# Kernel tuning notes

Measured on AMD Instinct MI355X. Metric: run time of the kernel, lower is better.

## Reference

```python
import jax, jax.numpy as jnp
import numpy as np

ALPHA = 500.0
BETA = 0.5
DEGREE = 20
LAMBDA_MAX = 100.0
N_USERS = 50000
N_ITEMS = 20000
NNZ = 2_000_000
BATCH = 128


def _aspire_filter(lam):
    exponent = 2.0 - BETA
    lam_pow = np.power(np.maximum(lam, 0.0), exponent / 2.0)
    return lam_pow / (lam_pow + ALPHA)


def _compute_chebyshev_coeffs(lambda_min, lambda_max, K):
    j = np.arange(K + 1)
    theta = np.pi * (j + 0.5) / (K + 1)
    t_nodes = np.cos(theta)
    mid, half = (lambda_max + lambda_min) / 2.0, (lambda_max - lambda_min) / 2.0
    f_nodes = _aspire_filter(mid + half * t_nodes)
    coeffs = np.zeros(K + 1)
    for k in range(K + 1):
        coeffs[k] = 2.0 / (K + 1) * np.sum(f_nodes * np.cos(k * theta))
    coeffs[0] /= 2.0
    return coeffs.astype(np.float32)


def setup_inputs() -> dict:
    key = jax.random.key(0)
    k1, k2, k3, k4 = jax.random.split(key, 4)
    rows = jax.random.randint(k1, (NNZ,), 0, N_USERS).astype(jnp.int32)
    cols = jax.random.randint(k2, (NNZ,), 0, N_ITEMS).astype(jnp.int32)
    vals = jax.random.uniform(k3, (NNZ,), dtype=jnp.float32)
    X_batch = jax.random.normal(k4, (BATCH, N_ITEMS), dtype=jnp.float32)
    coeffs = jnp.asarray(_compute_chebyshev_coeffs(0.0, LAMBDA_MAX, DEGREE))
    t_mid = jnp.full((1,), LAMBDA_MAX / 2.0, dtype=jnp.float32)
    t_half = jnp.full((1,), LAMBDA_MAX / 2.0, dtype=jnp.float32)
    return {
        "X_batch": X_batch,
        "vals": vals,
        "coeffs": coeffs,
        "t_mid": t_mid,
        "t_half": t_half,
        "rows": rows,
        "cols": cols,
        "n_users": N_USERS,
    }


def reference(X_batch, vals, coeffs, t_mid, t_half, rows, cols, n_users):
    n_items = X_batch.shape[1]

    def S_mapped(v):  # v: [n_items, batch]
        # X @ v : gather item rows, scatter-add into users
        u = jax.ops.segment_sum(vals[:, None] * v[cols], rows, num_segments=n_users)
        # X^T @ u : gather user rows, scatter-add into items
        w = jax.ops.segment_sum(vals[:, None] * u[rows], cols, num_segments=n_items)
        return (w - t_mid * v) / t_half

    T_prev = X_batch.T  # [n_items, batch]
    T_curr = S_mapped(T_prev)
    out0 = coeffs[0] * T_prev + coeffs[1] * T_curr

    def step(carry, c):
        Tp, Tc, acc = carry
        Tn = 2.0 * S_mapped(Tc) - Tp
        return (Tc, Tn, acc + c * Tn), None

    (_, _, out), _ = jax.lax.scan(step, (T_prev, T_curr, out0), coeffs[2:])
    return out.T  # [batch, n_items]
```

## Files before the change

### kernel.cpp

```cpp
#include <hip/hip_runtime.h>

#define BATCH 128
#define NUSERS 50000

__global__ void hist_k(const int* __restrict__ keys, int* __restrict__ hist, int nnz) {
  int i = blockIdx.x * blockDim.x + threadIdx.x;
  int st = gridDim.x * blockDim.x;
  for (; i < nnz; i += st) atomicAdd(&hist[keys[i]], 1);
}

__global__ void scan_k(const int* __restrict__ hist, int* __restrict__ offs,
                       int* __restrict__ cursor, int n) {
  __shared__ int wsum[16];
  __shared__ int carry;
  int tid = threadIdx.x;
  int lane = tid & 63;
  int wv = tid >> 6;
  if (tid == 0) carry = 0;
  __syncthreads();
  for (int base = 0; base < n; base += 1024) {
    int i = base + tid;
    int x = (i < n) ? hist[i] : 0;
    int incl = x;
#pragma unroll
    for (int d = 1; d < 64; d <<= 1) {
      int y = __shfl_up(incl, (unsigned)d, 64);
      if (lane >= d) incl += y;
    }
    if (lane == 63) wsum[wv] = incl;
    __syncthreads();
    if (wv == 0) {
      int t = (lane < 16) ? wsum[lane] : 0;
#pragma unroll
      for (int d = 1; d < 16; d <<= 1) {
        int y = __shfl_up(t, (unsigned)d, 64);
        if (lane >= d) t += y;
      }
      if (lane < 16) wsum[lane] = t;
    }
    __syncthreads();
    int woff = (wv > 0) ? wsum[wv - 1] : 0;
    int excl = carry + woff + incl - x;
    if (i < n) { offs[i] = excl; cursor[i] = excl; }
    int chunk_total = wsum[15];
    __syncthreads();
    if (tid == 0) carry += chunk_total;
    __syncthreads();
  }
  if (tid == 0) offs[n] = carry;
}

__global__ void scatter_k(const int* __restrict__ keys, const int* __restrict__ other,
                          const float* __restrict__ vals, int* __restrict__ cursor,
                          int2* __restrict__ out_ev, int nnz) {
  int i = blockIdx.x * blockDim.x + threadIdx.x;
  int st = gridDim.x * blockDim.x;
  for (; i < nnz; i += st) {
    int k = keys[i];
    int p = atomicAdd(&cursor[k], 1);
    out_ev[p] = make_int2(other[i], __float_as_int(vals[i]));
  }
}

__global__ void transpose_init_k(const float* __restrict__ Xb, const float* __restrict__ coeffs,
                                 float* __restrict__ T0, float* __restrict__ acc, int nitems) {
  __shared__ float tile[32][33];
  int tx = threadIdx.x, ty = threadIdx.y;
  int i0 = blockIdx.x * 32, b0 = blockIdx.y * 32;
#pragma unroll
  for (int j = 0; j < 4; j++) {
    int b = b0 + ty + j * 8;
    tile[ty + j * 8][tx] = Xb[(size_t)b * nitems + i0 + tx];
  }
  __syncthreads();
  float c0 = coeffs[0];
#pragma unroll
  for (int j = 0; j < 4; j++) {
    int il = ty + j * 8;
    float v = tile[tx][il];
    size_t idx = (size_t)(i0 + il) * BATCH + b0 + tx;
    T0[idx] = v;
    acc[idx] = c0 * v;
  }
}

__global__ void transpose_out_k(const float* __restrict__ acc, float* __restrict__ out, int nitems) {
  __shared__ float tile[32][33];
  int tx = threadIdx.x, ty = threadIdx.y;
  int i0 = blockIdx.x * 32, b0 = blockIdx.y * 32;
#pragma unroll
  for (int j = 0; j < 4; j++) {
    int il = ty + j * 8;
    tile[il][tx] = acc[(size_t)(i0 + il) * BATCH + b0 + tx];
  }
  __syncthreads();
#pragma unroll
  for (int j = 0; j < 4; j++) {
    int bl = ty + j * 8;
    out[(size_t)(b0 + bl) * nitems + i0 + tx] = tile[tx][bl];
  }
}

__global__ void __launch_bounds__(256) spmm_u_k(const int* __restrict__ offs,
                                                const int2* __restrict__ ev,
                                                const float* __restrict__ v,
                                                float* __restrict__ u, int nrows) {
  int row = (blockIdx.x << 2) | (threadIdx.x >> 6);
  if (row >= nrows) return;
  int lane = threadIdx.x & 63;
  int k0 = offs[row], k1 = offs[row + 1];
  float2 a0 = {0.f, 0.f}, a1 = {0.f, 0.f}, a2 = {0.f, 0.f}, a3 = {0.f, 0.f};
  int k = k0;
  int co = lane << 1;
  for (; k + 4 <= k1; k += 4) {
    int2 e0 = ev[k], e1 = ev[k + 1], e2 = ev[k + 2], e3 = ev[k + 3];
    float2 x0 = *reinterpret_cast<const float2*>(v + ((size_t)e0.x << 7) + co);
    float2 x1 = *reinterpret_cast<const float2*>(v + ((size_t)e1.x << 7) + co);
    float2 x2 = *reinterpret_cast<const float2*>(v + ((size_t)e2.x << 7) + co);
    float2 x3 = *reinterpret_cast<const float2*>(v + ((size_t)e3.x << 7) + co);
    float w0 = __int_as_float(e0.y), w1 = __int_as_float(e1.y);
    float w2 = __int_as_float(e2.y), w3 = __int_as_float(e3.y);
    a0.x = fmaf(w0, x0.x, a0.x); a0.y = fmaf(w0, x0.y, a0.y);
    a1.x = fmaf(w1, x1.x, a1.x); a1.y = fmaf(w1, x1.y, a1.y);
    a2.x = fmaf(w2, x2.x, a2.x); a2.y = fmaf(w2, x2.y, a2.y);
    a3.x = fmaf(w3, x3.x, a3.x); a3.y = fmaf(w3, x3.y, a3.y);
  }
  for (; k < k1; ++k) {
    int2 e = ev[k];
    float2 x = *reinterpret_cast<const float2*>(v + ((size_t)e.x << 7) + co);
    float w = __int_as_float(e.y);
    a0.x = fmaf(w, x.x, a0.x); a0.y = fmaf(w, x.y, a0.y);
  }
  float2 s;
  s.x = (a0.x + a1.x) + (a2.x + a3.x);
  s.y = (a0.y + a1.y) + (a2.y + a3.y);
  *reinterpret_cast<float2*>(u + ((size_t)row << 7) + co) = s;
}

__global__ void __launch_bounds__(256) spmm_i_cheb_k(const int* __restrict__ offs,
                                                     const int2* __restrict__ ev,
                                                     const float* __restrict__ u,
                                                     const float* __restrict__ vcur,
                                                     float* __restrict__ tio,
                                                     float* __restrict__ acc,
                                                     const float* __restrict__ t_mid,
                                                     const float* __restrict__ t_half,
                                                     const float* __restrict__ coeffs,
                                                     int cix, float sA, float sB, int nitems) {
  int item = (blockIdx.x << 2) | (threadIdx.x >> 6);
  if (item >= nitems) return;
  int lane = threadIdx.x & 63;
  int k0 = offs[item], k1 = offs[item + 1];
  float2 a0 = {0.f, 0.f}, a1 = {0.f, 0.f}, a2 = {0.f, 0.f}, a3 = {0.f, 0.f};
  int k = k0;
  int co = lane << 1;
  for (; k + 4 <= k1; k += 4) {
    int2 e0 = ev[k], e1 = ev[k + 1], e2 = ev[k + 2], e3 = ev[k + 3];
    float2 x0 = *reinterpret_cast<const float2*>(u + ((size_t)e0.x << 7) + co);
    float2 x1 = *reinterpret_cast<const float2*>(u + ((size_t)e1.x << 7) + co);
    float2 x2 = *reinterpret_cast<const float2*>(u + ((size_t)e2.x << 7) + co);
    float2 x3 = *reinterpret_cast<const float2*>(u + ((size_t)e3.x << 7) + co);
    float w0 = __int_as_float(e0.y), w1 = __int_as_float(e1.y);
    float w2 = __int_as_float(e2.y), w3 = __int_as_float(e3.y);
    a0.x = fmaf(w0, x0.x, a0.x); a0.y = fmaf(w0, x0.y, a0.y);
    a1.x = fmaf(w1, x1.x, a1.x); a1.y = fmaf(w1, x1.y, a1.y);
    a2.x = fmaf(w2, x2.x, a2.x); a2.y = fmaf(w2, x2.y, a2.y);
    a3.x = fmaf(w3, x3.x, a3.x); a3.y = fmaf(w3, x3.y, a3.y);
  }
  for (; k < k1; ++k) {
    int2 e = ev[k];
    float2 x = *reinterpret_cast<const float2*>(u + ((size_t)e.x << 7) + co);
    float w = __int_as_float(e.y);
    a0.x = fmaf(w, x.x, a0.x); a0.y = fmaf(w, x.y, a0.y);
  }
  float2 w;
  w.x = (a0.x + a1.x) + (a2.x + a3.x);
  w.y = (a0.y + a1.y) + (a2.y + a3.y);

  float mid = t_mid[0];
  float inv = 1.0f / t_half[0];
  float c = coeffs[cix];
  size_t idx = ((size_t)item << 7) + co;
  float2 vv = *reinterpret_cast<const float2*>(vcur + idx);
  float2 t;
  t.x = (w.x - mid * vv.x) * inv;
  t.y = (w.y - mid * vv.y) * inv;
  if (sB != 0.0f) {
    float2 p = *reinterpret_cast<const float2*>(tio + idx);
    t.x = sA * t.x - sB * p.x;
    t.y = sA * t.y - sB * p.y;
  }
  *reinterpret_cast<float2*>(tio + idx) = t;
  float2 a = *reinterpret_cast<const float2*>(acc + idx);
  a.x = fmaf(c, t.x, a.x);
  a.y = fmaf(c, t.y, a.y);
  *reinterpret_cast<float2*>(acc + idx) = a;
}

extern "C" void kernel_launch(void* const* d_in, const int* in_sizes, int n_in,
                              void* d_out, int out_size, void* d_ws, size_t ws_size,
                              hipStream_t stream) {
  const float* Xb     = (const float*)d_in[0];
  const float* vals   = (const float*)d_in[1];
  const float* coeffs = (const float*)d_in[2];
  const float* t_mid  = (const float*)d_in[3];
  const float* t_half = (const float*)d_in[4];
  const int*   rows   = (const int*)d_in[5];
  const int*   cols   = (const int*)d_in[6];

  int nnz    = in_sizes[1];
  int nitems = in_sizes[0] / BATCH;
  int nusers = NUSERS;
  int ncoef  = in_sizes[2];

  char* base = (char*)d_ws;
  size_t o = 0;
  auto alloc = [&](size_t bytes) -> void* {
    void* p = base + o;
    o = (o + bytes + 255) & ~(size_t)255;
    return p;
  };
  int2*  csr_ev   = (int2*)alloc((size_t)nnz * 8);
  int*   csr_offs = (int*)alloc((size_t)(nusers + 1) * 4);
  int2*  csc_ev   = (int2*)alloc((size_t)nnz * 8);
  int*   csc_offs = (int*)alloc((size_t)(nitems + 1) * 4);
  int*   cursor   = (int*)alloc((size_t)(nusers + 1) * 4);
  int*   hist     = (int*)alloc((size_t)(nusers + 1) * 4);
  float* u        = (float*)alloc((size_t)nusers * BATCH * 4);
  float* Ta       = (float*)alloc((size_t)nitems * BATCH * 4);
  float* Tb       = (float*)alloc((size_t)nitems * BATCH * 4);
  float* accb     = (float*)alloc((size_t)nitems * BATCH * 4);
  (void)ws_size;

  hipMemsetAsync(hist, 0, (size_t)(nusers + 1) * 4, stream);
  hist_k<<<2048, 256, 0, stream>>>(rows, hist, nnz);
  scan_k<<<1, 1024, 0, stream>>>(hist, csr_offs, cursor, nusers);
  scatter_k<<<2048, 256, 0, stream>>>(rows, cols, vals, cursor, csr_ev, nnz);

  hipMemsetAsync(hist, 0, (size_t)(nusers + 1) * 4, stream);
  hist_k<<<2048, 256, 0, stream>>>(cols, hist, nnz);
  scan_k<<<1, 1024, 0, stream>>>(hist, csc_offs, cursor, nitems);
  scatter_k<<<2048, 256, 0, stream>>>(cols, rows, vals, cursor, csc_ev, nnz);

  dim3 tb(32, 8);
  transpose_init_k<<<dim3(nitems / 32, BATCH / 32), tb, 0, stream>>>(Xb, coeffs, Ta, accb, nitems);

  int ublocks = (nusers + 3) / 4;
  int iblocks = (nitems + 3) / 4;

  spmm_u_k<<<ublocks, 256, 0, stream>>>(csr_offs, csr_ev, Ta, u, nusers);
  spmm_i_cheb_k<<<iblocks, 256, 0, stream>>>(csc_offs, csc_ev, u, Ta, Tb, accb,
                                             t_mid, t_half, coeffs, 1, 1.0f, 0.0f, nitems);
  float* Tp = Ta;
  float* Tc = Tb;
  for (int s = 2; s < ncoef; ++s) {
    spmm_u_k<<<ublocks, 256, 0, stream>>>(csr_offs, csr_ev, Tc, u, nusers);
    spmm_i_cheb_k<<<iblocks, 256, 0, stream>>>(csc_offs, csc_ev, u, Tc, Tp, accb,
                                               t_mid, t_half, coeffs, s, 2.0f, 1.0f, nitems);
    float* tmp = Tp; Tp = Tc; Tc = tmp;
  }

  transpose_out_k<<<dim3(nitems / 32, BATCH / 32), tb, 0, stream>>>(accb, (float*)d_out, nitems);
}
```

Measured before the change: 5.400 ms.

## Build CSR from CSC and rebuild CSC from CSR for locality, prefetch edges

The CSR is now built by rescattering a column-sorted COO, so each user's edges end up ordered by item. The CSC is then rebuilt from that CSR so each item's edges are ordered by user. Neighbouring gathers in the SpMM kernels should hit nearby rows of the dense operand, which improves cache locality. The SpMM loops also software-prefetch the next four edge entries and make the wave index uniform with readfirstlane. The cost is more preprocessing passes with atomics, plus reuse of the u buffer as scratch during setup.

Result: faster. 5.054 ms (-6.4%).

```diff
diff --git a/kernel.cpp b/kernel.cpp
--- a/kernel.cpp
+++ b/kernel.cpp
@@ -50,15 +50,34 @@
   if (tid == 0) offs[n] = carry;
 }
 
-__global__ void scatter_k(const int* __restrict__ keys, const int* __restrict__ other,
-                          const float* __restrict__ vals, int* __restrict__ cursor,
-                          int2* __restrict__ out_ev, int nnz) {
+__global__ void reinit_cursor_k(const int* __restrict__ offs, int* __restrict__ cursor, int n) {
+  int i = blockIdx.x * blockDim.x + threadIdx.x;
+  if (i < n) cursor[i] = offs[i];
+}
+
+__global__ void scatter1_k(const int* __restrict__ rows, const int* __restrict__ cols,
+                           const float* __restrict__ vals, int* __restrict__ cursor,
+                           int2* __restrict__ out_ev, int* __restrict__ keycomp, int nnz) {
   int i = blockIdx.x * blockDim.x + threadIdx.x;
   int st = gridDim.x * blockDim.x;
   for (; i < nnz; i += st) {
-    int k = keys[i];
-    int p = atomicAdd(&cursor[k], 1);
-    out_ev[p] = make_int2(other[i], __float_as_int(vals[i]));
+    int c = cols[i];
+    int p = atomicAdd(&cursor[c], 1);
+    out_ev[p] = make_int2(rows[i], __float_as_int(vals[i]));
+    keycomp[p] = c;
+  }
+}
+
+__global__ void rescatter_k(const int2* __restrict__ in_ev, const int* __restrict__ in_comp,
+                            int* __restrict__ cursor, int2* __restrict__ out_ev,
+                            int* __restrict__ out_comp, int nnz) {
+  int i = blockIdx.x * blockDim.x + threadIdx.x;
+  int st = gridDim.x * blockDim.x;
+  for (; i < nnz; i += st) {
+    int2 e = in_ev[i];
+    int q = atomicAdd(&cursor[e.x], 1);
+    out_ev[q] = make_int2(in_comp[i], e.y);
+    if (out_comp) out_comp[q] = e.x;
   }
 }
 
@@ -105,21 +124,27 @@
                                                 const int2* __restrict__ ev,
                                                 const float* __restrict__ v,
                                                 float* __restrict__ u, int nrows) {
-  int row = (blockIdx.x << 2) | (threadIdx.x >> 6);
+  int wid = __builtin_amdgcn_readfirstlane(threadIdx.x >> 6);
+  int row = (blockIdx.x << 2) | wid;
   if (row >= nrows) return;
   int lane = threadIdx.x & 63;
+  int co = lane << 1;
   int k0 = offs[row], k1 = offs[row + 1];
   float2 a0 = {0.f, 0.f}, a1 = {0.f, 0.f}, a2 = {0.f, 0.f}, a3 = {0.f, 0.f};
   int k = k0;
-  int co = lane << 1;
-  for (; k + 4 <= k1; k += 4) {
-    int2 e0 = ev[k], e1 = ev[k + 1], e2 = ev[k + 2], e3 = ev[k + 3];
+  int2 e0, e1, e2, e3;
+  bool have = (k + 4 <= k1);
+  if (have) { e0 = ev[k]; e1 = ev[k + 1]; e2 = ev[k + 2]; e3 = ev[k + 3]; }
+  while (have) {
     float2 x0 = *reinterpret_cast<const float2*>(v + ((size_t)e0.x << 7) + co);
     float2 x1 = *reinterpret_cast<const float2*>(v + ((size_t)e1.x << 7) + co);
     float2 x2 = *reinterpret_cast<const float2*>(v + ((size_t)e2.x << 7) + co);
     float2 x3 = *reinterpret_cast<const float2*>(v + ((size_t)e3.x << 7) + co);
     float w0 = __int_as_float(e0.y), w1 = __int_as_float(e1.y);
     float w2 = __int_as_float(e2.y), w3 = __int_as_float(e3.y);
+    k += 4;
+    have = (k + 4 <= k1);
+    if (have) { e0 = ev[k]; e1 = ev[k + 1]; e2 = ev[k + 2]; e3 = ev[k + 3]; }
     a0.x = fmaf(w0, x0.x, a0.x); a0.y = fmaf(w0, x0.y, a0.y);
     a1.x = fmaf(w1, x1.x, a1.x); a1.y = fmaf(w1, x1.y, a1.y);
     a2.x = fmaf(w2, x2.x, a2.x); a2.y = fmaf(w2, x2.y, a2.y);
@@ -147,21 +172,27 @@
                                                      const float* __restrict__ t_half,
                                                      const float* __restrict__ coeffs,
                                                      int cix, float sA, float sB, int nitems) {
-  int item = (blockIdx.x << 2) | (threadIdx.x >> 6);
+  int wid = __builtin_amdgcn_readfirstlane(threadIdx.x >> 6);
+  int item = (blockIdx.x << 2) | wid;
   if (item >= nitems) return;
   int lane = threadIdx.x & 63;
+  int co = lane << 1;
   int k0 = offs[item], k1 = offs[item + 1];
   float2 a0 = {0.f, 0.f}, a1 = {0.f, 0.f}, a2 = {0.f, 0.f}, a3 = {0.f, 0.f};
   int k = k0;
-  int co = lane << 1;
-  for (; k + 4 <= k1; k += 4) {
-    int2 e0 = ev[k], e1 = ev[k + 1], e2 = ev[k + 2], e3 = ev[k + 3];
+  int2 e0, e1, e2, e3;
+  bool have = (k + 4 <= k1);
+  if (have) { e0 = ev[k]; e1 = ev[k + 1]; e2 = ev[k + 2]; e3 = ev[k + 3]; }
+  while (have) {
     float2 x0 = *reinterpret_cast<const float2*>(u + ((size_t)e0.x << 7) + co);
     float2 x1 = *reinterpret_cast<const float2*>(u + ((size_t)e1.x << 7) + co);
     float2 x2 = *reinterpret_cast<const float2*>(u + ((size_t)e2.x << 7) + co);
     float2 x3 = *reinterpret_cast<const float2*>(u + ((size_t)e3.x << 7) + co);
     float w0 = __int_as_float(e0.y), w1 = __int_as_float(e1.y);
     float w2 = __int_as_float(e2.y), w3 = __int_as_float(e3.y);
+    k += 4;
+    have = (k + 4 <= k1);
+    if (have) { e0 = ev[k]; e1 = ev[k + 1]; e2 = ev[k + 2]; e3 = ev[k + 3]; }
     a0.x = fmaf(w0, x0.x, a0.x); a0.y = fmaf(w0, x0.y, a0.y);
     a1.x = fmaf(w1, x1.x, a1.x); a1.y = fmaf(w1, x1.y, a1.y);
     a2.x = fmaf(w2, x2.x, a2.x); a2.y = fmaf(w2, x2.y, a2.y);
@@ -220,9 +251,9 @@
     o = (o + bytes + 255) & ~(size_t)255;
     return p;
   };
+  int2*  csc_ev   = (int2*)alloc((size_t)nnz * 8);
   int2*  csr_ev   = (int2*)alloc((size_t)nnz * 8);
   int*   csr_offs = (int*)alloc((size_t)(nusers + 1) * 4);
-  int2*  csc_ev   = (int2*)alloc((size_t)nnz * 8);
   int*   csc_offs = (int*)alloc((size_t)(nitems + 1) * 4);
   int*   cursor   = (int*)alloc((size_t)(nusers + 1) * 4);
   int*   hist     = (int*)alloc((size_t)(nusers + 1) * 4);
@@ -231,16 +262,22 @@
   float* Tb       = (float*)alloc((size_t)nitems * BATCH * 4);
   float* accb     = (float*)alloc((size_t)nitems * BATCH * 4);
   (void)ws_size;
+  int* comp_a = (int*)u;
+  int* comp_b = ((int*)u) + nnz;
+
+  hipMemsetAsync(hist, 0, (size_t)(nusers + 1) * 4, stream);
+  hist_k<<<2048, 256, 0, stream>>>(cols, hist, nnz);
+  scan_k<<<1, 1024, 0, stream>>>(hist, csc_offs, cursor, nitems);
+  int2* csc_tmp = csc_ev;
+  scatter1_k<<<2048, 256, 0, stream>>>(rows, cols, vals, cursor, csc_tmp, comp_a, nnz);
 
   hipMemsetAsync(hist, 0, (size_t)(nusers + 1) * 4, stream);
   hist_k<<<2048, 256, 0, stream>>>(rows, hist, nnz);
   scan_k<<<1, 1024, 0, stream>>>(hist, csr_offs, cursor, nusers);
-  scatter_k<<<2048, 256, 0, stream>>>(rows, cols, vals, cursor, csr_ev, nnz);
-
-  hipMemsetAsync(hist, 0, (size_t)(nusers + 1) * 4, stream);
-  hist_k<<<2048, 256, 0, stream>>>(cols, hist, nnz);
-  scan_k<<<1, 1024, 0, stream>>>(hist, csc_offs, cursor, nitems);
-  scatter_k<<<2048, 256, 0, stream>>>(cols, rows, vals, cursor, csc_ev, nnz);
+  rescatter_k<<<2048, 256, 0, stream>>>(csc_tmp, comp_a, cursor, csr_ev, comp_b, nnz);
+
+  reinit_cursor_k<<<(nitems + 255) / 256, 256, 0, stream>>>(csc_offs, cursor, nitems);
+  rescatter_k<<<2048, 256, 0, stream>>>(csr_ev, comp_b, cursor, csc_ev, (int*)nullptr, nnz);
 
   dim3 tb(32, 8);
   transpose_init_k<<<dim3(nitems / 32, BATCH / 32), tb, 0, stream>>>(Xb, coeffs, Ta, accb, nitems);
```

## Split batch into 16-column slices and map 8 lanes per row in SpMM

Applied to the files above, without the earlier changes.

Dense operands are re-laid out as eight 16-wide batch slices, so each SpMM block works on one slice and the gathered rows form a working set small enough for cache. Each row is handled by 8 lanes that share edge indices through shuffles, replacing one 64-lane wavefront per row, which raises parallelism for short rows. CSR and CSC construction are also fused into single histogram and scatter passes. The cost is eight times more gather passes over the edge lists, each fetching only 64-byte segments.

Result: faster. 4.896 ms (-9.3%).

```diff
diff --git a/kernel.cpp b/kernel.cpp
--- a/kernel.cpp
+++ b/kernel.cpp
@@ -2,11 +2,17 @@
 
 #define BATCH 128
 #define NUSERS 50000
-
-__global__ void hist_k(const int* __restrict__ keys, int* __restrict__ hist, int nnz) {
+#define PW 16
+#define NSL 8
+
+__global__ void hist2_k(const int* __restrict__ rows, const int* __restrict__ cols,
+                        int* __restrict__ histU, int* __restrict__ histI, int nnz) {
   int i = blockIdx.x * blockDim.x + threadIdx.x;
   int st = gridDim.x * blockDim.x;
-  for (; i < nnz; i += st) atomicAdd(&hist[keys[i]], 1);
+  for (; i < nnz; i += st) {
+    atomicAdd(&histU[rows[i]], 1);
+    atomicAdd(&histI[cols[i]], 1);
+  }
 }
 
 __global__ void scan_k(const int* __restrict__ hist, int* __restrict__ offs,
@@ -50,91 +56,76 @@
   if (tid == 0) offs[n] = carry;
 }
 
-__global__ void scatter_k(const int* __restrict__ keys, const int* __restrict__ other,
-                          const float* __restrict__ vals, int* __restrict__ cursor,
-                          int2* __restrict__ out_ev, int nnz) {
+__global__ void scatter2_k(const int* __restrict__ rows, const int* __restrict__ cols,
+                           const float* __restrict__ vals, int* __restrict__ curU,
+                           int* __restrict__ curI, int2* __restrict__ csr_ev,
+                           int2* __restrict__ csc_ev, int nnz) {
   int i = blockIdx.x * blockDim.x + threadIdx.x;
   int st = gridDim.x * blockDim.x;
   for (; i < nnz; i += st) {
-    int k = keys[i];
-    int p = atomicAdd(&cursor[k], 1);
-    out_ev[p] = make_int2(other[i], __float_as_int(vals[i]));
+    int r = rows[i], c = cols[i];
+    int vb = __float_as_int(vals[i]);
+    int p = atomicAdd(&curU[r], 1);
+    csr_ev[p] = make_int2(c, vb);
+    int q = atomicAdd(&curI[c], 1);
+    csc_ev[q] = make_int2(r, vb);
   }
 }
 
 __global__ void transpose_init_k(const float* __restrict__ Xb, const float* __restrict__ coeffs,
                                  float* __restrict__ T0, float* __restrict__ acc, int nitems) {
-  __shared__ float tile[32][33];
+  __shared__ float t[16][17];
   int tx = threadIdx.x, ty = threadIdx.y;
-  int i0 = blockIdx.x * 32, b0 = blockIdx.y * 32;
-#pragma unroll
-  for (int j = 0; j < 4; j++) {
-    int b = b0 + ty + j * 8;
-    tile[ty + j * 8][tx] = Xb[(size_t)b * nitems + i0 + tx];
-  }
+  int p = blockIdx.y;
+  int i0 = blockIdx.x * 16;
+  t[ty][tx] = Xb[(size_t)(p * 16 + ty) * nitems + i0 + tx];
   __syncthreads();
   float c0 = coeffs[0];
-#pragma unroll
-  for (int j = 0; j < 4; j++) {
-    int il = ty + j * 8;
-    float v = tile[tx][il];
-    size_t idx = (size_t)(i0 + il) * BATCH + b0 + tx;
-    T0[idx] = v;
-    acc[idx] = c0 * v;
-  }
+  float v = t[tx][ty];
+  size_t o = (size_t)p * nitems * PW + (size_t)(i0 + ty) * PW + tx;
+  T0[o] = v;
+  acc[o] = c0 * v;
 }
 
 __global__ void transpose_out_k(const float* __restrict__ acc, float* __restrict__ out, int nitems) {
-  __shared__ float tile[32][33];
+  __shared__ float t[16][17];
   int tx = threadIdx.x, ty = threadIdx.y;
-  int i0 = blockIdx.x * 32, b0 = blockIdx.y * 32;
-#pragma unroll
-  for (int j = 0; j < 4; j++) {
-    int il = ty + j * 8;
-    tile[il][tx] = acc[(size_t)(i0 + il) * BATCH + b0 + tx];
-  }
+  int p = blockIdx.y;
+  int i0 = blockIdx.x * 16;
+  t[ty][tx] = acc[(size_t)p * nitems * PW + (size_t)(i0 + ty) * PW + tx];
   __syncthreads();
-#pragma unroll
-  for (int j = 0; j < 4; j++) {
-    int bl = ty + j * 8;
-    out[(size_t)(b0 + bl) * nitems + i0 + tx] = tile[tx][bl];
-  }
+  out[(size_t)(p * 16 + ty) * nitems + i0 + tx] = t[tx][ty];
 }
 
 __global__ void __launch_bounds__(256) spmm_u_k(const int* __restrict__ offs,
                                                 const int2* __restrict__ ev,
                                                 const float* __restrict__ v,
-                                                float* __restrict__ u, int nrows) {
-  int row = (blockIdx.x << 2) | (threadIdx.x >> 6);
+                                                float* __restrict__ u,
+                                                int nrows, size_t vstride, size_t ustride) {
+  int s = blockIdx.x & 7;
+  int g = blockIdx.x >> 3;
+  int slot = threadIdx.x >> 3;
+  int lane8 = threadIdx.x & 7;
+  int row = g * 32 + slot;
   if (row >= nrows) return;
-  int lane = threadIdx.x & 63;
   int k0 = offs[row], k1 = offs[row + 1];
-  float2 a0 = {0.f, 0.f}, a1 = {0.f, 0.f}, a2 = {0.f, 0.f}, a3 = {0.f, 0.f};
-  int k = k0;
-  int co = lane << 1;
-  for (; k + 4 <= k1; k += 4) {
-    int2 e0 = ev[k], e1 = ev[k + 1], e2 = ev[k + 2], e3 = ev[k + 3];
-    float2 x0 = *reinterpret_cast<const float2*>(v + ((size_t)e0.x << 7) + co);
-    float2 x1 = *reinterpret_cast<const float2*>(v + ((size_t)e1.x << 7) + co);
-    float2 x2 = *reinterpret_cast<const float2*>(v + ((size_t)e2.x << 7) + co);
-    float2 x3 = *reinterpret_cast<const float2*>(v + ((size_t)e3.x << 7) + co);
-    float w0 = __int_as_float(e0.y), w1 = __int_as_float(e1.y);
-    float w2 = __int_as_float(e2.y), w3 = __int_as_float(e3.y);
-    a0.x = fmaf(w0, x0.x, a0.x); a0.y = fmaf(w0, x0.y, a0.y);
-    a1.x = fmaf(w1, x1.x, a1.x); a1.y = fmaf(w1, x1.y, a1.y);
-    a2.x = fmaf(w2, x2.x, a2.x); a2.y = fmaf(w2, x2.y, a2.y);
-    a3.x = fmaf(w3, x3.x, a3.x); a3.y = fmaf(w3, x3.y, a3.y);
-  }
-  for (; k < k1; ++k) {
-    int2 e = ev[k];
-    float2 x = *reinterpret_cast<const float2*>(v + ((size_t)e.x << 7) + co);
-    float w = __int_as_float(e.y);
-    a0.x = fmaf(w, x.x, a0.x); a0.y = fmaf(w, x.y, a0.y);
-  }
-  float2 s;
-  s.x = (a0.x + a1.x) + (a2.x + a3.x);
-  s.y = (a0.y + a1.y) + (a2.y + a3.y);
-  *reinterpret_cast<float2*>(u + ((size_t)row << 7) + co) = s;
+  const float* vp = v + (size_t)s * vstride + (lane8 << 1);
+  float2 a = {0.f, 0.f};
+  int base = threadIdx.x & ~7;
+  for (int k = k0; k < k1; k += 8) {
+    int kk = k + lane8;
+    int2 e = (kk < k1) ? ev[kk] : make_int2(0, 0);
+#pragma unroll
+    for (int j = 0; j < 8; j++) {
+      int src = base | j;
+      int idx = __shfl(e.x, src);
+      float w = __int_as_float(__shfl(e.y, src));
+      float2 x = *reinterpret_cast<const float2*>(vp + ((size_t)idx << 4));
+      a.x = fmaf(w, x.x, a.x);
+      a.y = fmaf(w, x.y, a.y);
+    }
+  }
+  *reinterpret_cast<float2*>(u + (size_t)s * ustride + ((size_t)row << 4) + (lane8 << 1)) = a;
 }
 
 __global__ void __launch_bounds__(256) spmm_i_cheb_k(const int* __restrict__ offs,
@@ -146,41 +137,35 @@
                                                      const float* __restrict__ t_mid,
                                                      const float* __restrict__ t_half,
                                                      const float* __restrict__ coeffs,
-                                                     int cix, float sA, float sB, int nitems) {
-  int item = (blockIdx.x << 2) | (threadIdx.x >> 6);
+                                                     int cix, float sA, float sB,
+                                                     int nitems, size_t ustride, size_t tstride) {
+  int s = blockIdx.x & 7;
+  int g = blockIdx.x >> 3;
+  int slot = threadIdx.x >> 3;
+  int lane8 = threadIdx.x & 7;
+  int item = g * 32 + slot;
   if (item >= nitems) return;
-  int lane = threadIdx.x & 63;
   int k0 = offs[item], k1 = offs[item + 1];
-  float2 a0 = {0.f, 0.f}, a1 = {0.f, 0.f}, a2 = {0.f, 0.f}, a3 = {0.f, 0.f};
-  int k = k0;
-  int co = lane << 1;
-  for (; k + 4 <= k1; k += 4) {
-    int2 e0 = ev[k], e1 = ev[k + 1], e2 = ev[k + 2], e3 = ev[k + 3];
-    float2 x0 = *reinterpret_cast<const float2*>(u + ((size_t)e0.x << 7) + co);
-    float2 x1 = *reinterpret_cast<const float2*>(u + ((size_t)e1.x << 7) + co);
-    float2 x2 = *reinterpret_cast<const float2*>(u + ((size_t)e2.x << 7) + co);
-    float2 x3 = *reinterpret_cast<const float2*>(u + ((size_t)e3.x << 7) + co);
-    float w0 = __int_as_float(e0.y), w1 = __int_as_float(e1.y);
-    float w2 = __int_as_float(e2.y), w3 = __int_as_float(e3.y);
-    a0.x = fmaf(w0, x0.x, a0.x); a0.y = fmaf(w0, x0.y, a0.y);
-    a1.x = fmaf(w1, x1.x, a1.x); a1.y = fmaf(w1, x1.y, a1.y);
-    a2.x = fmaf(w2, x2.x, a2.x); a2.y = fmaf(w2, x2.y, a2.y);
-    a3.x = fmaf(w3, x3.x, a3.x); a3.y = fmaf(w3, x3.y, a3.y);
-  }
-  for (; k < k1; ++k) {
-    int2 e = ev[k];
-    float2 x = *reinterpret_cast<const float2*>(u + ((size_t)e.x << 7) + co);
-    float w = __int_as_float(e.y);
-    a0.x = fmaf(w, x.x, a0.x); a0.y = fmaf(w, x.y, a0.y);
-  }
-  float2 w;
-  w.x = (a0.x + a1.x) + (a2.x + a3.x);
-  w.y = (a0.y + a1.y) + (a2.y + a3.y);
-
+  const float* up = u + (size_t)s * ustride + (lane8 << 1);
+  float2 w = {0.f, 0.f};
+  int base = threadIdx.x & ~7;
+  for (int k = k0; k < k1; k += 8) {
+    int kk = k + lane8;
+    int2 e = (kk < k1) ? ev[kk] : make_int2(0, 0);
+#pragma unroll
+    for (int j = 0; j < 8; j++) {
+      int src = base | j;
+      int idx = __shfl(e.x, src);
+      float wv = __int_as_float(__shfl(e.y, src));
+      float2 x = *reinterpret_cast<const float2*>(up + ((size_t)idx << 4));
+      w.x = fmaf(wv, x.x, w.x);
+      w.y = fmaf(wv, x.y, w.y);
+    }
+  }
   float mid = t_mid[0];
   float inv = 1.0f / t_half[0];
   float c = coeffs[cix];
-  size_t idx = ((size_t)item << 7) + co;
+  size_t idx = (size_t)s * tstride + ((size_t)item << 4) + (lane8 << 1);
   float2 vv = *reinterpret_cast<const float2*>(vcur + idx);
   float2 t;
   t.x = (w.x - mid * vv.x) * inv;
@@ -213,6 +198,9 @@
   int nusers = NUSERS;
   int ncoef  = in_sizes[2];
 
+  size_t vstride = (size_t)nitems * PW;
+  size_t ustride = (size_t)nusers * PW;
+
   char* base = (char*)d_ws;
   size_t o = 0;
   auto alloc = [&](size_t bytes) -> void* {
@@ -221,44 +209,45 @@
     return p;
   };
   int2*  csr_ev   = (int2*)alloc((size_t)nnz * 8);
+  int2*  csc_ev   = (int2*)alloc((size_t)nnz * 8);
   int*   csr_offs = (int*)alloc((size_t)(nusers + 1) * 4);
-  int2*  csc_ev   = (int2*)alloc((size_t)nnz * 8);
   int*   csc_offs = (int*)alloc((size_t)(nitems + 1) * 4);
-  int*   cursor   = (int*)alloc((size_t)(nusers + 1) * 4);
-  int*   hist     = (int*)alloc((size_t)(nusers + 1) * 4);
-  float* u        = (float*)alloc((size_t)nusers * BATCH * 4);
-  float* Ta       = (float*)alloc((size_t)nitems * BATCH * 4);
-  float* Tb       = (float*)alloc((size_t)nitems * BATCH * 4);
-  float* accb     = (float*)alloc((size_t)nitems * BATCH * 4);
+  int*   curU     = (int*)alloc((size_t)(nusers + 1) * 4);
+  int*   curI     = (int*)alloc((size_t)(nitems + 1) * 4);
+  int*   histU    = (int*)alloc((size_t)(nusers + 1) * 4);
+  int*   histI    = (int*)alloc((size_t)(nitems + 1) * 4);
+  float* u        = (float*)alloc((size_t)NSL * ustride * 4);
+  float* Ta       = (float*)alloc((size_t)NSL * vstride * 4);
+  float* Tb       = (float*)alloc((size_t)NSL * vstride * 4);
+  float* accb     = (float*)alloc((size_t)NSL * vstride * 4);
   (void)ws_size;
 
-  hipMemsetAsync(hist, 0, (size_t)(nusers + 1) * 4, stream);
-  hist_k<<<2048, 256, 0, stream>>>(rows, hist, nnz);
-  scan_k<<<1, 1024, 0, stream>>>(hist, csr_offs, cursor, nusers);
-  scatter_k<<<2048, 256, 0, stream>>>(rows, cols, vals, cursor, csr_ev, nnz);
-
-  hipMemsetAsync(hist, 0, (size_t)(nusers + 1) * 4, stream);
-  hist_k<<<2048, 256, 0, stream>>>(cols, hist, nnz);
-  scan_k<<<1, 1024, 0, stream>>>(hist, csc_offs, cursor, nitems);
-  scatter_k<<<2048, 256, 0, stream>>>(cols, rows, vals, cursor, csc_ev, nnz);
-
-  dim3 tb(32, 8);
-  transpose_init_k<<<dim3(nitems / 32, BATCH / 32), tb, 0, stream>>>(Xb, coeffs, Ta, accb, nitems);
-
-  int ublocks = (nusers + 3) / 4;
-  int iblocks = (nitems + 3) / 4;
-
-  spmm_u_k<<<ublocks, 256, 0, stream>>>(csr_offs, csr_ev, Ta, u, nusers);
+  hipMemsetAsync(histU, 0, (size_t)(nusers + 1) * 4, stream);
+  hipMemsetAsync(histI, 0, (size_t)(nitems + 1) * 4, stream);
+  hist2_k<<<2048, 256, 0, stream>>>(rows, cols, histU, histI, nnz);
+  scan_k<<<1, 1024, 0, stream>>>(histU, csr_offs, curU, nusers);
+  scan_k<<<1, 1024, 0, stream>>>(histI, csc_offs, curI, nitems);
+  scatter2_k<<<2048, 256, 0, stream>>>(rows, cols, vals, curU, curI, csr_ev, csc_ev, nnz);
+
+  dim3 tb16(16, 16);
+  transpose_init_k<<<dim3(nitems / 16, BATCH / 16), tb16, 0, stream>>>(Xb, coeffs, Ta, accb, nitems);
+
+  int ublocks = ((nusers + 31) / 32) * NSL;
+  int iblocks = ((nitems + 31) / 32) * NSL;
+
+  spmm_u_k<<<ublocks, 256, 0, stream>>>(csr_offs, csr_ev, Ta, u, nusers, vstride, ustride);
   spmm_i_cheb_k<<<iblocks, 256, 0, stream>>>(csc_offs, csc_ev, u, Ta, Tb, accb,
-                                             t_mid, t_half, coeffs, 1, 1.0f, 0.0f, nitems);
+                                             t_mid, t_half, coeffs, 1, 1.0f, 0.0f,
+                                             nitems, ustride, vstride);
   float* Tp = Ta;
   float* Tc = Tb;
   for (int s = 2; s < ncoef; ++s) {
-    spmm_u_k<<<ublocks, 256, 0, stream>>>(csr_offs, csr_ev, Tc, u, nusers);
+    spmm_u_k<<<ublocks, 256, 0, stream>>>(csr_offs, csr_ev, Tc, u, nusers, vstride, ustride);
     spmm_i_cheb_k<<<iblocks, 256, 0, stream>>>(csc_offs, csc_ev, u, Tc, Tp, accb,
-                                               t_mid, t_half, coeffs, s, 2.0f, 1.0f, nitems);
+                                               t_mid, t_half, coeffs, s, 2.0f, 1.0f,
+                                               nitems, ustride, vstride);
     float* tmp = Tp; Tp = Tc; Tc = tmp;
   }
 
-  transpose_out_k<<<dim3(nitems / 32, BATCH / 32), tb, 0, stream>>>(accb, (float*)d_out, nitems);
-}
+  transpose_out_k<<<dim3(nitems / 16, BATCH / 16), tb16, 0, stream>>>(accb, (float*)d_out, nitems);
+}
```
